# Optimization experiments

Measured on AMD Instinct MI355X. Metric: run time of the kernel, lower is better.

The kernel has to match this reference:

```python
import jax, jax.numpy as jnp
import numpy as np
import math

B, S, H, D = 8, 2048, 1024, 64  # batch, seq_len, hidden_dim, head_size

def setup_inputs() -> dict:
    key = jax.random.key(0)
    ks = jax.random.split(key, 7)
    lim = 1.0 / math.sqrt(H)  # torch Linear default init bound
    return {
        "x":  jax.random.normal(ks[0], (B, S, H), dtype=jnp.float32),
        "Wq": jax.random.uniform(ks[1], (H, D), jnp.float32, -lim, lim),
        "bq": jax.random.uniform(ks[2], (D,),   jnp.float32, -lim, lim),
        "Wk": jax.random.uniform(ks[3], (H, D), jnp.float32, -lim, lim),
        "bk": jax.random.uniform(ks[4], (D,),   jnp.float32, -lim, lim),
        "Wv": jax.random.uniform(ks[5], (H, D), jnp.float32, -lim, lim),
        "bv": jax.random.uniform(ks[6], (D,),   jnp.float32, -lim, lim),
    }

def reference(x, Wq, bq, Wk, bk, Wv, bv):
    # x: [B, S, H]
    q = x @ Wq + bq          # [B, S, D]
    k = x @ Wk + bk          # [B, S, D]
    v = x @ Wv + bv          # [B, S, D]
    scores = jnp.einsum("bsd,btd->bst", q, k)       # [B, S, S]
    causal = jnp.tril(jnp.ones((S, S), dtype=bool))
    scores = jnp.where(causal, scores, -jnp.inf)
    # NOTE: original module (faithfully) applies softmax FIRST, then divides
    # by sqrt(hidden_dim) -- it does NOT scale logits before softmax.
    weight = jax.nn.softmax(scores, axis=-1) / jnp.sqrt(jnp.float32(x.shape[-1]))
    # dropout p=0.0 -> identity
    return jnp.einsum("bst,btd->bsd", weight, v)     # [B, S, D]
```

## Files before the change

kernel.cpp:

```cpp
#include <hip/hip_runtime.h>


typedef float     f32x4 __attribute__((ext_vector_type(4)));
typedef _Float16  f16x8 __attribute__((ext_vector_type(8)));
typedef _Float16  f16x4 __attribute__((ext_vector_type(4)));

template<bool V> struct BoolT { static constexpr bool value = V; };

__global__ __launch_bounds__(256) void wt_prep(const float* __restrict__ Wq,
                                               const float* __restrict__ Wk,
                                               const float* __restrict__ Wv,
                                               _Float16* __restrict__ WtF) {
  const int w  = blockIdx.x >> 4;
  const int kt = blockIdx.x & 15;
  const float* src = (w == 0) ? Wq : (w == 1 ? Wk : Wv);
  __shared__ _Float16 ls[64][72];
  const int t = threadIdx.x;
  {
    int rr = t >> 4;
    int c4 = (t & 15) * 4;
    #pragma unroll
    for (int ri = 0; ri < 4; ++ri) {
      int k = rr + ri * 16;
      f32x4 f = *(const f32x4*)&src[(size_t)(kt * 64 + k) * 64 + c4];
      #pragma unroll
      for (int j = 0; j < 4; ++j) ls[k][c4 + j] = (_Float16)f[j];
    }
  }
  __syncthreads();
  const int lane = t & 63, l16 = lane & 15, quad = lane >> 4;
  #pragma unroll
  for (int h = 0; h < 2; ++h) {
    int fid     = h * 4 + (t >> 6);
    int kstep_l = fid >> 2;
    int ntl     = fid & 3;
    int nt      = w * 4 + ntl;
    int kstep   = kt * 2 + kstep_l;
    f16x8 o;
    #pragma unroll
    for (int j = 0; j < 8; ++j) o[j] = ls[kstep_l * 32 + quad * 8 + j][ntl * 16 + l16];
    *(f16x8*)&WtF[((size_t)(kstep * 12 + nt) * 64 + lane) * 8] = o;
  }
}

__global__ __launch_bounds__(512, 4) void qkv_gemm(const float* __restrict__ x,
                                                   const _Float16* __restrict__ WtF,
                                                   const float* __restrict__ bq,
                                                   const float* __restrict__ bk,
                                                   const float* __restrict__ bv,
                                                   _Float16* __restrict__ qo,
                                                   _Float16* __restrict__ ko,
                                                   _Float16* __restrict__ vt) {
  __shared__ _Float16 xs[32 * 1024];
  const int tid  = threadIdx.x;
  const int wave = tid >> 6, lane = tid & 63;
  const int l16  = lane & 15, quad = lane >> 4;
  const int mhalf = wave >> 2;
  const int ngrp  = wave & 3;
  const int bid   = blockIdx.x;
  const int m0    = (((bid & 7) << 6) + (bid >> 3)) * 32;

  {
    int row   = tid >> 4;
    int cbase = (tid & 15) * 4;
    const float* xrow = x + (size_t)(m0 + row) * 1024;
    int key = row & 7;
    #pragma unroll
    for (int j = 0; j < 16; ++j) {
      int col = cbase + j * 64;
      f32x4 f = *(const f32x4*)&xrow[col];
      f16x4 hh;
      #pragma unroll
      for (int e = 0; e < 4; ++e) hh[e] = (_Float16)f[e];
      int g   = col >> 3;
      int sub = col & 7;
      *(f16x4*)&xs[(size_t)row * 1024 + (size_t)((g ^ key) << 3) + sub] = hh;
    }
  }
  __syncthreads();

  f32x4 acc0 = (f32x4){0.f,0.f,0.f,0.f};
  f32x4 acc1 = (f32x4){0.f,0.f,0.f,0.f};
  f32x4 acc2 = (f32x4){0.f,0.f,0.f,0.f};

  const int arow = mhalf * 16 + l16;
  const _Float16* abase = xs + (size_t)arow * 1024;
  const int akey = arow & 7;
  const _Float16* wbase = WtF + ((size_t)(ngrp * 3) * 64 + lane) * 8;

  #pragma unroll 4
  for (int kstep = 0; kstep < 32; ++kstep) {
    f16x8 a = *(const f16x8*)(abase + (((kstep * 4 + quad) ^ akey) << 3));
    const _Float16* wk = wbase + (size_t)kstep * (12 * 64 * 8);
    f16x8 b0 = *(const f16x8*)(wk);
    f16x8 b1 = *(const f16x8*)(wk + 512);
    f16x8 b2 = *(const f16x8*)(wk + 1024);
    acc0 = __builtin_amdgcn_mfma_f32_16x16x32_f16(a, b0, acc0, 0, 0, 0);
    acc1 = __builtin_amdgcn_mfma_f32_16x16x32_f16(a, b1, acc1, 0, 0, 0);
    acc2 = __builtin_amdgcn_mfma_f32_16x16x32_f16(a, b2, acc2, 0, 0, 0);
  }

  f32x4 accs[3] = {acc0, acc1, acc2};
  #pragma unroll
  for (int i = 0; i < 3; ++i) {
    int nt  = ngrp * 3 + i;
    int col = nt * 16 + l16;
    float bias = (nt < 4) ? bq[col] : (nt < 8) ? bk[col - 64] : bv[col - 128];
    #pragma unroll
    for (int r = 0; r < 4; ++r) {
      int m = m0 + mhalf * 16 + quad * 4 + r;
      _Float16 hv = (_Float16)(accs[i][r] + bias);
      if (nt < 4)      qo[(size_t)m * 64 + col] = hv;
      else if (nt < 8) ko[(size_t)m * 64 + (col - 64)] = hv;
      else {
        int b = m >> 11, s = m & 2047;
        vt[((size_t)b * 64 + (col - 128)) * 2048 + s] = hv;
      }
    }
  }
}

__global__ __launch_bounds__(512, 2) void attn(const _Float16* __restrict__ q,
                                               const _Float16* __restrict__ k,
                                               const _Float16* __restrict__ vt,
                                               float* __restrict__ out) {
  const int blk  = blockIdx.x;
  const int pair = blk >> 3;
  const int b    = blk & 7;
  const int tid  = threadIdx.x;
  const int wave = tid >> 6, lane = tid & 63;
  const int l16  = lane & 15, quad = lane >> 4;
  const int wv   = wave & 3;
  const int half = wave >> 2;
  const int qt   = half ? (127 - pair) : pair;
  const int q0   = qt * 16;

  __shared__ _Float16 P[8][16][136];
  __shared__ float    ob[8][16][68];
  __shared__ float    mlb[8][2][16];

  const _Float16* qb = q  + (size_t)b * 2048 * 64;
  const _Float16* kb = k  + (size_t)b * 2048 * 64;
  const _Float16* vb = vt + (size_t)b * 64 * 2048;

  f16x8 qf0 = *(const f16x8*)&qb[(q0 + l16) * 64 + quad * 8];
  f16x8 qf1 = *(const f16x8*)&qb[(q0 + l16) * 64 + 32 + quad * 8];

  f32x4 o[4];
  #pragma unroll
  for (int i = 0; i < 4; ++i) o[i] = (f32x4){0.f, 0.f, 0.f, 0.f};
  float m = -1e30f, l = 0.f;
  const float L2E = 1.44269504088896340736f;
  const int qrow  = q0 + l16;
  const int kvend = q0 + 16;

  auto chunk = [&](int kv0, auto fullc) {
    constexpr bool FULL = decltype(fullc)::value;

    f16x8 kf[8][2];
    #pragma unroll
    for (int t = 0; t < 8; ++t) {
      if (FULL || kv0 + t * 16 < kvend) {
        kf[t][0] = *(const f16x8*)&kb[(kv0 + t * 16 + l16) * 64 + quad * 8];
        kf[t][1] = *(const f16x8*)&kb[(kv0 + t * 16 + l16) * 64 + 32 + quad * 8];
      }
    }
    f16x8 vf[4][4];
    #pragma unroll
    for (int ks = 0; ks < 4; ++ks) {
      if (FULL || kv0 + ks * 32 < kvend) {
        #pragma unroll
        for (int dt = 0; dt < 4; ++dt)
          vf[ks][dt] = *(const f16x8*)&vb[(size_t)(dt * 16 + l16) * 2048 + kv0 + ks * 32 + quad * 8];
      }
    }

    f32x4 sc[8];
    #pragma unroll
    for (int t = 0; t < 8; ++t) {
      int kvc = kv0 + t * 16;
      f32x4 c;
      if (FULL || kvc < kvend) {
        c = (f32x4){0.f, 0.f, 0.f, 0.f};
        c = __builtin_amdgcn_mfma_f32_16x16x32_f16(kf[t][0], qf0, c, 0, 0, 0);
        c = __builtin_amdgcn_mfma_f32_16x16x32_f16(kf[t][1], qf1, c, 0, 0, 0);
        if (kvc + 15 > q0) {
          #pragma unroll
          for (int r = 0; r < 4; ++r)
            if (kvc + quad * 4 + r > qrow) c[r] = -1e30f;
        }
      } else {
        c = (f32x4){-1e30f, -1e30f, -1e30f, -1e30f};
      }
      sc[t] = c;
    }

    float mx = -1e30f;
    #pragma unroll
    for (int t = 0; t < 8; ++t)
      mx = fmaxf(mx, fmaxf(fmaxf(sc[t][0], sc[t][1]), fmaxf(sc[t][2], sc[t][3])));
    mx = fmaxf(mx, __shfl_xor(mx, 16, 64));
    mx = fmaxf(mx, __shfl_xor(mx, 32, 64));
    float mnew  = fmaxf(m, mx);
    float alpha = exp2f((m - mnew) * L2E);
    m = mnew;

    float s = 0.f;
    #pragma unroll
    for (int t = 0; t < 8; ++t) {
      #pragma unroll
      for (int r = 0; r < 4; ++r) sc[t][r] = exp2f((sc[t][r] - m) * L2E);
      s += (sc[t][0] + sc[t][1]) + (sc[t][2] + sc[t][3]);
    }
    s += __shfl_xor(s, 16, 64);
    s += __shfl_xor(s, 32, 64);
    l = l * alpha + s;
    #pragma unroll
    for (int dt = 0; dt < 4; ++dt)
      #pragma unroll
      for (int r = 0; r < 4; ++r) o[dt][r] *= alpha;

    #pragma unroll
    for (int t = 0; t < 8; ++t) {
      f16x4 ph;
      #pragma unroll
      for (int r = 0; r < 4; ++r) ph[r] = (_Float16)sc[t][r];
      *(f16x4*)&P[wave][l16][t * 16 + quad * 4] = ph;
    }
    asm volatile("s_waitcnt lgkmcnt(0)" ::: "memory");

    #pragma unroll
    for (int ks = 0; ks < 4; ++ks) {
      if (FULL || kv0 + ks * 32 < kvend) {
        f16x8 pf = *(const f16x8*)&P[wave][l16][ks * 32 + quad * 8];
        #pragma unroll
        for (int dt = 0; dt < 4; ++dt)
          o[dt] = __builtin_amdgcn_mfma_f32_16x16x32_f16(vf[ks][dt], pf, o[dt], 0, 0, 0);
      }
    }
  };

  for (int kv0 = wv * 128; kv0 < kvend; kv0 += 512) {
    if (kv0 + 128 <= kvend) chunk(kv0, BoolT<true>{});
    else                    chunk(kv0, BoolT<false>{});
  }

  #pragma unroll
  for (int dt = 0; dt < 4; ++dt)
    *(f32x4*)&ob[wave][l16][dt * 16 + quad * 4] = o[dt];
  if (quad == 0) {
    mlb[wave][0][l16] = m;
    mlb[wave][1][l16] = l;
  }
  __syncthreads();

  {
    int mhalf = tid >> 8;
    int idx   = tid & 255;
    int row   = idx >> 4;
    int c0    = (idx & 15) * 4;
    int wbase = mhalf * 4;
    int qth   = mhalf ? (127 - pair) : pair;
    float m0 = mlb[wbase + 0][0][row], m1 = mlb[wbase + 1][0][row];
    float m2 = mlb[wbase + 2][0][row], m3 = mlb[wbase + 3][0][row];
    float M  = fmaxf(fmaxf(m0, m1), fmaxf(m2, m3));
    float w0 = exp2f((m0 - M) * L2E), w1 = exp2f((m1 - M) * L2E);
    float w2 = exp2f((m2 - M) * L2E), w3 = exp2f((m3 - M) * L2E);
    float L  = w0 * mlb[wbase + 0][1][row] + w1 * mlb[wbase + 1][1][row]
             + w2 * mlb[wbase + 2][1][row] + w3 * mlb[wbase + 3][1][row];
    float inv = 1.0f / (L * 32.0f);
    f32x4 res;
    #pragma unroll
    for (int j = 0; j < 4; ++j)
      res[j] = (w0 * ob[wbase + 0][row][c0 + j] + w1 * ob[wbase + 1][row][c0 + j]
              + w2 * ob[wbase + 2][row][c0 + j] + w3 * ob[wbase + 3][row][c0 + j]) * inv;
    *(f32x4*)&out[((size_t)b * 2048 + qth * 16 + row) * 64 + c0] = res;
  }
}

extern "C" void kernel_launch(void* const* d_in, const int* in_sizes, int n_in,
                              void* d_out, int out_size, void* d_ws, size_t ws_size,
                              hipStream_t stream) {
  const float* x  = (const float*)d_in[0];
  const float* Wq = (const float*)d_in[1];
  const float* bq = (const float*)d_in[2];
  const float* Wk = (const float*)d_in[3];
  const float* bk = (const float*)d_in[4];
  const float* Wv = (const float*)d_in[5];
  const float* bv = (const float*)d_in[6];
  float* out = (float*)d_out;

  _Float16* WtF = (_Float16*)d_ws;
  _Float16* qo  = WtF + 192 * 1024;
  _Float16* ko  = qo + 16384 * 64;
  _Float16* vt  = ko + 16384 * 64;

  hipLaunchKernelGGL(wt_prep,  dim3(48),  dim3(256), 0, stream, Wq, Wk, Wv, WtF);
  hipLaunchKernelGGL(qkv_gemm, dim3(512), dim3(512), 0, stream, x, WtF, bq, bk, bv, qo, ko, vt);
  hipLaunchKernelGGL(attn,     dim3(512), dim3(512), 0, stream, qo, ko, vt, out);
}
```

Baseline: 158.4 us.

## Split causal attention into per-chunk partial kernel plus separate merge kernel

Replaces the fused attention kernel, where each block handled a pair of query tiles with 4 waves striding over KV chunks, with a flash-decoding-style split. Each wave now computes exactly one (query tile, 128-wide KV chunk) work item and writes its unnormalized partial output plus max and sum to global memory. A second kernel merges the partials per query tile. This is meant to balance the triangular causal workload evenly across many small work items. In exchange it adds roughly 35 MB of extra global writes and reads, plus an extra kernel launch.

```diff
diff --git a/kernel.cpp b/kernel.cpp
--- a/kernel.cpp
+++ b/kernel.cpp
@@ -120,24 +120,38 @@
   }
 }
 
-__global__ __launch_bounds__(512, 2) void attn(const _Float16* __restrict__ q,
-                                               const _Float16* __restrict__ k,
-                                               const _Float16* __restrict__ vt,
-                                               float* __restrict__ out) {
-  const int blk  = blockIdx.x;
-  const int pair = blk >> 3;
-  const int b    = blk & 7;
+__global__ __launch_bounds__(256, 3) void attn_part(const _Float16* __restrict__ q,
+                                                    const _Float16* __restrict__ k,
+                                                    const _Float16* __restrict__ vt,
+                                                    float* __restrict__ po,
+                                                    float* __restrict__ pml) {
   const int tid  = threadIdx.x;
   const int wave = tid >> 6, lane = tid & 63;
   const int l16  = lane & 15, quad = lane >> 4;
-  const int wv   = wave & 3;
-  const int half = wave >> 2;
-  const int qt   = half ? (127 - pair) : pair;
-  const int q0   = qt * 16;
-
-  __shared__ _Float16 P[8][16][136];
-  __shared__ float    ob[8][16][68];
-  __shared__ float    mlb[8][2][16];
+  const int item = blockIdx.x * 4 + wave;
+
+  const int b = item / 1088;
+  const int r = item - b * 1088;
+  int g = 0;
+  {
+    int lo = 0, hi = 16;
+    while (lo < hi) {
+      int mid = (lo + hi + 1) >> 1;
+      if (4 * mid * (mid + 1) <= r) lo = mid; else hi = mid - 1;
+    }
+    g = lo;
+  }
+  const int rr    = r - 4 * g * (g + 1);
+  const int n     = g + 1;
+  const int tile  = rr / n;
+  const int c     = rr - tile * n;
+  const int qt    = 8 * g + tile;
+  const int q0    = qt * 16;
+  const int kv0   = c * 128;
+  const int kvlen = min(128, q0 + 16 - kv0);
+
+  __shared__ _Float16 P[4][16][136];
+  __shared__ float    ob[4][16][68];
 
   const _Float16* qb = q  + (size_t)b * 2048 * 64;
   const _Float16* kb = k  + (size_t)b * 2048 * 64;
@@ -146,53 +160,49 @@
   f16x8 qf0 = *(const f16x8*)&qb[(q0 + l16) * 64 + quad * 8];
   f16x8 qf1 = *(const f16x8*)&qb[(q0 + l16) * 64 + 32 + quad * 8];
 
-  f32x4 o[4];
-  #pragma unroll
-  for (int i = 0; i < 4; ++i) o[i] = (f32x4){0.f, 0.f, 0.f, 0.f};
-  float m = -1e30f, l = 0.f;
   const float L2E = 1.44269504088896340736f;
   const int qrow  = q0 + l16;
-  const int kvend = q0 + 16;
-
-  auto chunk = [&](int kv0, auto fullc) {
+
+  float m, l;
+  f32x4 o[4];
+
+  auto body = [&](auto fullc) {
     constexpr bool FULL = decltype(fullc)::value;
 
     f16x8 kf[8][2];
     #pragma unroll
-    for (int t = 0; t < 8; ++t) {
-      if (FULL || kv0 + t * 16 < kvend) {
+    for (int t = 0; t < 8; ++t)
+      if (FULL || t * 16 < kvlen) {
         kf[t][0] = *(const f16x8*)&kb[(kv0 + t * 16 + l16) * 64 + quad * 8];
         kf[t][1] = *(const f16x8*)&kb[(kv0 + t * 16 + l16) * 64 + 32 + quad * 8];
       }
-    }
     f16x8 vf[4][4];
     #pragma unroll
-    for (int ks = 0; ks < 4; ++ks) {
-      if (FULL || kv0 + ks * 32 < kvend) {
+    for (int ks = 0; ks < 4; ++ks)
+      if (FULL || ks * 32 < kvlen) {
         #pragma unroll
         for (int dt = 0; dt < 4; ++dt)
           vf[ks][dt] = *(const f16x8*)&vb[(size_t)(dt * 16 + l16) * 2048 + kv0 + ks * 32 + quad * 8];
       }
-    }
 
     f32x4 sc[8];
     #pragma unroll
     for (int t = 0; t < 8; ++t) {
-      int kvc = kv0 + t * 16;
-      f32x4 c;
-      if (FULL || kvc < kvend) {
-        c = (f32x4){0.f, 0.f, 0.f, 0.f};
-        c = __builtin_amdgcn_mfma_f32_16x16x32_f16(kf[t][0], qf0, c, 0, 0, 0);
-        c = __builtin_amdgcn_mfma_f32_16x16x32_f16(kf[t][1], qf1, c, 0, 0, 0);
+      const int kvc = kv0 + t * 16;
+      f32x4 cc;
+      if (FULL || t * 16 < kvlen) {
+        cc = (f32x4){0.f, 0.f, 0.f, 0.f};
+        cc = __builtin_amdgcn_mfma_f32_16x16x32_f16(kf[t][0], qf0, cc, 0, 0, 0);
+        cc = __builtin_amdgcn_mfma_f32_16x16x32_f16(kf[t][1], qf1, cc, 0, 0, 0);
         if (kvc + 15 > q0) {
           #pragma unroll
-          for (int r = 0; r < 4; ++r)
-            if (kvc + quad * 4 + r > qrow) c[r] = -1e30f;
+          for (int rr2 = 0; rr2 < 4; ++rr2)
+            if (kvc + quad * 4 + rr2 > qrow) cc[rr2] = -1e30f;
         }
       } else {
-        c = (f32x4){-1e30f, -1e30f, -1e30f, -1e30f};
-      }
-      sc[t] = c;
+        cc = (f32x4){-1e30f, -1e30f, -1e30f, -1e30f};
+      }
+      sc[t] = cc;
     }
 
     float mx = -1e30f;
@@ -201,81 +211,88 @@
       mx = fmaxf(mx, fmaxf(fmaxf(sc[t][0], sc[t][1]), fmaxf(sc[t][2], sc[t][3])));
     mx = fmaxf(mx, __shfl_xor(mx, 16, 64));
     mx = fmaxf(mx, __shfl_xor(mx, 32, 64));
-    float mnew  = fmaxf(m, mx);
-    float alpha = exp2f((m - mnew) * L2E);
-    m = mnew;
+    m = mx;
 
     float s = 0.f;
     #pragma unroll
     for (int t = 0; t < 8; ++t) {
       #pragma unroll
-      for (int r = 0; r < 4; ++r) sc[t][r] = exp2f((sc[t][r] - m) * L2E);
+      for (int rr2 = 0; rr2 < 4; ++rr2) sc[t][rr2] = exp2f((sc[t][rr2] - m) * L2E);
       s += (sc[t][0] + sc[t][1]) + (sc[t][2] + sc[t][3]);
     }
     s += __shfl_xor(s, 16, 64);
     s += __shfl_xor(s, 32, 64);
-    l = l * alpha + s;
-    #pragma unroll
-    for (int dt = 0; dt < 4; ++dt)
-      #pragma unroll
-      for (int r = 0; r < 4; ++r) o[dt][r] *= alpha;
+    l = s;
 
     #pragma unroll
     for (int t = 0; t < 8; ++t) {
       f16x4 ph;
       #pragma unroll
-      for (int r = 0; r < 4; ++r) ph[r] = (_Float16)sc[t][r];
+      for (int rr2 = 0; rr2 < 4; ++rr2) ph[rr2] = (_Float16)sc[t][rr2];
       *(f16x4*)&P[wave][l16][t * 16 + quad * 4] = ph;
     }
     asm volatile("s_waitcnt lgkmcnt(0)" ::: "memory");
 
     #pragma unroll
-    for (int ks = 0; ks < 4; ++ks) {
-      if (FULL || kv0 + ks * 32 < kvend) {
+    for (int i = 0; i < 4; ++i) o[i] = (f32x4){0.f, 0.f, 0.f, 0.f};
+    #pragma unroll
+    for (int ks = 0; ks < 4; ++ks)
+      if (FULL || ks * 32 < kvlen) {
         f16x8 pf = *(const f16x8*)&P[wave][l16][ks * 32 + quad * 8];
         #pragma unroll
         for (int dt = 0; dt < 4; ++dt)
           o[dt] = __builtin_amdgcn_mfma_f32_16x16x32_f16(vf[ks][dt], pf, o[dt], 0, 0, 0);
       }
-    }
   };
-
-  for (int kv0 = wv * 128; kv0 < kvend; kv0 += 512) {
-    if (kv0 + 128 <= kvend) chunk(kv0, BoolT<true>{});
-    else                    chunk(kv0, BoolT<false>{});
-  }
+  if (kvlen == 128) body(BoolT<true>{});
+  else              body(BoolT<false>{});
 
   #pragma unroll
   for (int dt = 0; dt < 4; ++dt)
     *(f32x4*)&ob[wave][l16][dt * 16 + quad * 4] = o[dt];
   if (quad == 0) {
-    mlb[wave][0][l16] = m;
-    mlb[wave][1][l16] = l;
-  }
-  __syncthreads();
-
+    pml[(size_t)item * 32 + l16]      = m;
+    pml[(size_t)item * 32 + 16 + l16] = l;
+  }
+  asm volatile("s_waitcnt lgkmcnt(0)" ::: "memory");
   {
-    int mhalf = tid >> 8;
-    int idx   = tid & 255;
-    int row   = idx >> 4;
-    int c0    = (idx & 15) * 4;
-    int wbase = mhalf * 4;
-    int qth   = mhalf ? (127 - pair) : pair;
-    float m0 = mlb[wbase + 0][0][row], m1 = mlb[wbase + 1][0][row];
-    float m2 = mlb[wbase + 2][0][row], m3 = mlb[wbase + 3][0][row];
-    float M  = fmaxf(fmaxf(m0, m1), fmaxf(m2, m3));
-    float w0 = exp2f((m0 - M) * L2E), w1 = exp2f((m1 - M) * L2E);
-    float w2 = exp2f((m2 - M) * L2E), w3 = exp2f((m3 - M) * L2E);
-    float L  = w0 * mlb[wbase + 0][1][row] + w1 * mlb[wbase + 1][1][row]
-             + w2 * mlb[wbase + 2][1][row] + w3 * mlb[wbase + 3][1][row];
-    float inv = 1.0f / (L * 32.0f);
-    f32x4 res;
+    const int row = lane >> 2, c4 = (lane & 3) * 16;
+    float* dst = po + (size_t)item * 1024 + row * 64 + c4;
     #pragma unroll
     for (int j = 0; j < 4; ++j)
-      res[j] = (w0 * ob[wbase + 0][row][c0 + j] + w1 * ob[wbase + 1][row][c0 + j]
-              + w2 * ob[wbase + 2][row][c0 + j] + w3 * ob[wbase + 3][row][c0 + j]) * inv;
-    *(f32x4*)&out[((size_t)b * 2048 + qth * 16 + row) * 64 + c0] = res;
-  }
+      *(f32x4*)&dst[j * 4] = *(const f32x4*)&ob[wave][row][c4 + j * 4];
+  }
+}
+
+__global__ __launch_bounds__(256) void attn_merge(const float* __restrict__ po,
+                                                  const float* __restrict__ pml,
+                                                  float* __restrict__ out) {
+  const int blk = blockIdx.x;
+  const int b   = blk >> 7, qt = blk & 127;
+  const int g   = qt >> 3, n = g + 1;
+  const int base = b * 1088 + 4 * g * (g + 1) + (qt & 7) * n;
+  const int t   = threadIdx.x;
+  const int qr  = t >> 4, d0 = (t & 15) * 4;
+  const float L2E = 1.44269504088896340736f;
+
+  const float* mlp = pml + (size_t)base * 32 + qr;
+  float M = -1e30f;
+  for (int it = 0; it < n; ++it) M = fmaxf(M, mlp[it * 32]);
+
+  float L = 0.f;
+  f32x4 acc = (f32x4){0.f, 0.f, 0.f, 0.f};
+  for (int it = 0; it < n; ++it) {
+    float w = exp2f((mlp[it * 32] - M) * L2E);
+    L += w * mlp[it * 32 + 16];
+    f32x4 p = *(const f32x4*)&po[((size_t)(base + it) * 16 + qr) * 64 + d0];
+    #pragma unroll
+    for (int jj = 0; jj < 4; ++jj) acc[jj] += w * p[jj];
+  }
+  const float inv = 1.0f / (L * 32.0f);
+  f32x4 res;
+  #pragma unroll
+  for (int jj = 0; jj < 4; ++jj) res[jj] = acc[jj] * inv;
+  *(f32x4*)&out[((size_t)b * 2048 + qt * 16 + qr) * 64 + d0] = res;
 }
 
 extern "C" void kernel_launch(void* const* d_in, const int* in_sizes, int n_in,
@@ -294,8 +311,11 @@
   _Float16* qo  = WtF + 192 * 1024;
   _Float16* ko  = qo + 16384 * 64;
   _Float16* vt  = ko + 16384 * 64;
-
-  hipLaunchKernelGGL(wt_prep,  dim3(48),  dim3(256), 0, stream, Wq, Wk, Wv, WtF);
-  hipLaunchKernelGGL(qkv_gemm, dim3(512), dim3(512), 0, stream, x, WtF, bq, bk, bv, qo, ko, vt);
-  hipLaunchKernelGGL(attn,     dim3(512), dim3(512), 0, stream, qo, ko, vt, out);
-}
+  float*    po  = (float*)(vt + 8 * 64 * 2048);
+  float*    pml = po + (size_t)8704 * 1024;
+
+  hipLaunchKernelGGL(wt_prep,    dim3(48),   dim3(256), 0, stream, Wq, Wk, Wv, WtF);
+  hipLaunchKernelGGL(qkv_gemm,   dim3(512),  dim3(512), 0, stream, x, WtF, bq, bk, bv, qo, ko, vt);
+  hipLaunchKernelGGL(attn_part,  dim3(2176), dim3(256), 0, stream, qo, ko, vt, po, pml);
+  hipLaunchKernelGGL(attn_merge, dim3(1024), dim3(256), 0, stream, po, pml, out);
+}
```

Result: slower. 168.7 us (+6.5%).
